# Kernel optimization log

Hardware: AMD Instinct MI355X
Metric: run time of the kernel (lower is better)

## Reference

```python
import jax, jax.numpy as jnp
import numpy as np

TEMPERATURE = 0.07
EPS = 1e-8          # torch cosine_similarity norm clamp
DIAG_FILL = 9e-15   # value masked_fill'ed onto the diagonal BEFORE temperature scaling


def setup_inputs() -> dict:
    key = jax.random.key(0)
    N, D = 16384, 128
    feats = jax.random.normal(key, (N, D), dtype=jnp.float32)
    # unique labels: required for the original torch code's broadcast
    # (-cos_sim[pos_mask] must have exactly N elements)
    labels = jnp.arange(N, dtype=jnp.int32).reshape(N, 1)
    return {"feats": feats, "labels": labels}


def reference(feats, labels):
    # cosine similarity matrix: normalize rows once, then a single GEMM
    norm = jnp.maximum(jnp.linalg.norm(feats, axis=-1, keepdims=True), EPS)
    f = feats / norm
    cos_sim = f @ f.T                                   # [N, N]

    N = cos_sim.shape[0]
    eye = jnp.eye(N, dtype=bool)
    cos_sim = jnp.where(eye, DIAG_FILL, cos_sim)        # masked_fill_(self_mask, 9e-15)
    cos_sim = cos_sim / TEMPERATURE

    pos_mask = labels == labels.T                       # [N, N] bool, one True per row
    # cos_sim[pos_mask] with exactly one positive per row == masked row-sum
    pos = jnp.sum(jnp.where(pos_mask, cos_sim, 0.0), axis=-1)  # [N]

    nll = -pos + jax.nn.logsumexp(cos_sim, axis=-1)     # [N]
    return jnp.mean(nll)
```

## Files before the change

kernel.cpp:

```cpp
#include <hip/hip_runtime.h>
#include <hip/hip_bf16.h>
#include <stdint.h>

typedef __attribute__((ext_vector_type(8))) short short8;
typedef __attribute__((ext_vector_type(4))) float f32x4;

#define N_ROWS 16384
#define DIM 128

constexpr float ALPHA = 4.5398160f;
constexpr float POSC = 1.2857143e-13f;

__device__ __forceinline__ void gload_lds16(const void* g, void* lds) {
  __builtin_amdgcn_global_load_lds(
      (const __attribute__((address_space(1))) void*)(uintptr_t)g,
      (__attribute__((address_space(3))) void*)(uintptr_t)lds,
      16, 0, 0);
}

__global__ void normalize_kernel(const float* __restrict__ feats,
                                 unsigned short* __restrict__ G,
                                 float* __restrict__ rowsum) {
  const int tid  = threadIdx.x;
  const int lane = tid & 63;
  const int row  = blockIdx.x * 4 + (tid >> 6);

  const float2 v = *(const float2*)(feats + (size_t)row * DIM + lane * 2);
  float ss = v.x * v.x + v.y * v.y;
#pragma unroll
  for (int m = 1; m < 64; m <<= 1) ss += __shfl_xor(ss, m);
  const float sc = ALPHA / fmaxf(sqrtf(ss), 1e-8f);

  __hip_bfloat16 h0 = __float2bfloat16(v.x * sc);
  __hip_bfloat16 h1 = __float2bfloat16(v.y * sc);
  unsigned int packed = (unsigned int)(*(unsigned short*)&h0) |
                        ((unsigned int)(*(unsigned short*)&h1) << 16);
  *(unsigned int*)(G + (size_t)row * DIM + lane * 2) = packed;

  if (blockIdx.x < 64) rowsum[blockIdx.x * 256 + tid] = 0.f;
}

__global__ __launch_bounds__(256, 2) void simclr_lse_kernel(
    const unsigned short* __restrict__ G, float* __restrict__ rowsum) {
  const int tid  = threadIdx.x;
  const int lane = tid & 63;
  const int w    = tid >> 6;
  const int wr   = w >> 1;
  const int wc   = w & 1;
  const int c    = lane & 15;
  const int q    = lane >> 4;

  const int rt      = blockIdx.x & 127;
  const int seg     = blockIdx.x >> 7;
  const int rowBase = rt * 128;

  __shared__ __align__(16) unsigned short Bbuf[128 * 128];
  __shared__ float ldsRow[128];

  if (tid < 128) ldsRow[tid] = 0.f;

  short8 afrag[4][4];
  {
    const short* Gs = (const short*)G;
    const int rbw = rowBase + wr * 64;
#pragma unroll
    for (int tr = 0; tr < 4; ++tr)
#pragma unroll
      for (int ks = 0; ks < 4; ++ks) {
        const int row = rbw + tr * 16 + c;
        afrag[tr][ks] = *(const short8*)(Gs + (size_t)row * DIM + ks * 32 + q * 8);
      }
  }

  unsigned boff[4][4];
#pragma unroll
  for (int tc = 0; tc < 4; ++tc)
#pragma unroll
    for (int ks = 0; ks < 4; ++ks) {
      const int col = wc * 64 + tc * 16 + c;
      const int kc  = ks * 4 + q;
      boff[tc][ks] = (unsigned)((col * 16 + (kc ^ c)) * 16);
    }

  unsigned goff[8];
#pragma unroll
  for (int t = 0; t < 8; ++t) {
    const int cidx = t * 256 + tid;
    const int col  = cidx >> 4;
    const int kc   = (cidx & 15) ^ (col & 15);
    goff[t] = (unsigned)(col * DIM + kc * 8);
  }

  float rs[4][4];
#pragma unroll
  for (int tr = 0; tr < 4; ++tr)
#pragma unroll
    for (int r = 0; r < 4; ++r) rs[tr][r] = 0.f;

  const f32x4 zero4 = {0.f, 0.f, 0.f, 0.f};
  const char* bbase = (const char*)Bbuf;

  for (int ch = 0; ch < 32; ++ch) {
    const int cb = seg * 4096 + ch * 128;
    __syncthreads();
    {
      const unsigned short* gsrc = G + (size_t)cb * DIM;
#pragma unroll
      for (int t = 0; t < 8; ++t)
        gload_lds16(gsrc + goff[t], (void*)(Bbuf + (size_t)(t * 256 + w * 64) * 8));
    }
    __syncthreads();

    f32x4 acc[4][4];
#pragma unroll
    for (int ks = 0; ks < 4; ++ks) {
      short8 bfr[4];
#pragma unroll
      for (int tc = 0; tc < 4; ++tc)
        bfr[tc] = *(const short8*)(bbase + boff[tc][ks]);
#pragma unroll
      for (int tr = 0; tr < 4; ++tr)
#pragma unroll
        for (int tc = 0; tc < 4; ++tc) {
          if (ks == 0)
            acc[tr][tc] = __builtin_amdgcn_mfma_f32_16x16x32_bf16(
                afrag[tr][0], bfr[tc], zero4, 0, 0, 0);
          else
            acc[tr][tc] = __builtin_amdgcn_mfma_f32_16x16x32_bf16(
                afrag[tr][ks], bfr[tc], acc[tr][tc], 0, 0, 0);
        }
    }

    if (cb == rowBase && wr == wc) {
#pragma unroll
      for (int tr = 0; tr < 4; ++tr)
#pragma unroll
        for (int r = 0; r < 4; ++r)
          if (c == q * 4 + r) acc[tr][tr][r] = 0.f;
    }

#pragma unroll
    for (int tr = 0; tr < 4; ++tr)
#pragma unroll
      for (int r = 0; r < 4; ++r) {
        float s = rs[tr][r];
#pragma unroll
        for (int tc = 0; tc < 4; ++tc)
          s += __builtin_amdgcn_exp2f(acc[tr][tc][r]);
        rs[tr][r] = s;
      }
  }

#pragma unroll
  for (int tr = 0; tr < 4; ++tr)
#pragma unroll
    for (int r = 0; r < 4; ++r) {
      float v = rs[tr][r];
      v += __shfl_xor(v, 1);
      v += __shfl_xor(v, 2);
      v += __shfl_xor(v, 4);
      v += __shfl_xor(v, 8);
      rs[tr][r] = v;
    }
  if (c == 0) {
#pragma unroll
    for (int tr = 0; tr < 4; ++tr)
#pragma unroll
      for (int r = 0; r < 4; ++r)
        atomicAdd(&ldsRow[wr * 64 + tr * 16 + q * 4 + r], rs[tr][r]);
  }
  __syncthreads();
  if (tid < 128) atomicAdd(&rowsum[rowBase + tid], ldsRow[tid]);
}

__global__ void finalize_kernel(const float* __restrict__ rowsum,
                                float* __restrict__ out) {
  const int tid = threadIdx.x;
  float local = 0.f;
  for (int i = tid; i < N_ROWS; i += 1024) local += logf(rowsum[i]);
#pragma unroll
  for (int m = 1; m < 64; m <<= 1) local += __shfl_xor(local, m);
  __shared__ float part[16];
  if ((tid & 63) == 0) part[tid >> 6] = local;
  __syncthreads();
  if (tid == 0) {
    float s = 0.f;
#pragma unroll
    for (int i = 0; i < 16; ++i) s += part[i];
    out[0] = s / (float)N_ROWS - POSC;
  }
}

extern "C" void kernel_launch(void* const* d_in, const int* in_sizes, int n_in,
                              void* d_out, int out_size, void* d_ws, size_t ws_size,
                              hipStream_t stream) {
  (void)in_sizes; (void)n_in; (void)out_size; (void)ws_size;
  const float* feats = (const float*)d_in[0];
  unsigned short* G = (unsigned short*)d_ws;
  float* rowsum = (float*)((char*)d_ws + (size_t)N_ROWS * DIM * 2);

  normalize_kernel<<<dim3(N_ROWS / 4), dim3(256), 0, stream>>>(feats, G, rowsum);
  simclr_lse_kernel<<<dim3(512), dim3(256), 0, stream>>>(G, rowsum);
  finalize_kernel<<<dim3(1), dim3(1024), 0, stream>>>(rowsum, d_out ? (float*)d_out : nullptr);
}
```

Before: 131.2 us.

## Exploit Gram symmetry with triangular tile scheduling and fuse finalize via last-block

Because the similarity matrix is symmetric, only upper-triangular 128x128 tiles are computed. Each off-diagonal tile's exponentials feed both row sums and column sums, which roughly halves the MFMA and exp work. Tiles are taken from a persistent grid through an atomic work counter in groups of four, and the A fragment is reused while the row tile stays the same. The separate finalize kernel is folded into the last finishing block using a completion counter, which removes a launch. This adds more atomics, extra column reductions through LDS, and a serial log-sum tail in a single block.

Result: slower. 362.2 us (+176.2%).

```diff
diff --git a/kernel.cpp b/kernel.cpp
--- a/kernel.cpp
+++ b/kernel.cpp
@@ -7,9 +7,13 @@
 
 #define N_ROWS 16384
 #define DIM 128
+#define NT 128
+#define TOTAL_CHUNKS 8256
+#define TRI_BLOCKS 1024
 
 constexpr float ALPHA = 4.5398160f;
-constexpr float POSC = 1.2857143e-13f;
+constexpr float POSC  = 1.2857143e-13f;
+constexpr float LN2   = 0.69314718056f;
 
 __device__ __forceinline__ void gload_lds16(const void* g, void* lds) {
   __builtin_amdgcn_global_load_lds(
@@ -20,7 +24,8 @@
 
 __global__ void normalize_kernel(const float* __restrict__ feats,
                                  unsigned short* __restrict__ G,
-                                 float* __restrict__ rowsum) {
+                                 float* __restrict__ rowsum,
+                                 unsigned int* __restrict__ cnts) {
   const int tid  = threadIdx.x;
   const int lane = tid & 63;
   const int row  = blockIdx.x * 4 + (tid >> 6);
@@ -38,49 +43,26 @@
   *(unsigned int*)(G + (size_t)row * DIM + lane * 2) = packed;
 
   if (blockIdx.x < 64) rowsum[blockIdx.x * 256 + tid] = 0.f;
-}
-
-__global__ __launch_bounds__(256, 2) void simclr_lse_kernel(
-    const unsigned short* __restrict__ G, float* __restrict__ rowsum) {
+  if (blockIdx.x == 0 && tid < 2) cnts[tid] = 0u;
+}
+
+__global__ __launch_bounds__(256, 3) void simclr_tri_kernel(
+    const unsigned short* __restrict__ G, float* __restrict__ rowsum,
+    unsigned int* __restrict__ cnts, float* __restrict__ out) {
   const int tid  = threadIdx.x;
   const int lane = tid & 63;
   const int w    = tid >> 6;
-  const int wr   = w >> 1;
-  const int wc   = w & 1;
   const int c    = lane & 15;
   const int q    = lane >> 4;
 
-  const int rt      = blockIdx.x & 127;
-  const int seg     = blockIdx.x >> 7;
-  const int rowBase = rt * 128;
-
   __shared__ __align__(16) unsigned short Bbuf[128 * 128];
-  __shared__ float ldsRow[128];
-
-  if (tid < 128) ldsRow[tid] = 0.f;
-
-  short8 afrag[4][4];
-  {
-    const short* Gs = (const short*)G;
-    const int rbw = rowBase + wr * 64;
-#pragma unroll
-    for (int tr = 0; tr < 4; ++tr)
-#pragma unroll
-      for (int ks = 0; ks < 4; ++ks) {
-        const int row = rbw + tr * 16 + c;
-        afrag[tr][ks] = *(const short8*)(Gs + (size_t)row * DIM + ks * 32 + q * 8);
-      }
-  }
-
-  unsigned boff[4][4];
-#pragma unroll
-  for (int tc = 0; tc < 4; ++tc)
-#pragma unroll
-    for (int ks = 0; ks < 4; ++ks) {
-      const int col = wc * 64 + tc * 16 + c;
-      const int kc  = ks * 4 + q;
-      boff[tc][ks] = (unsigned)((col * 16 + (kc ^ c)) * 16);
-    }
+  __shared__ float ldsCol[2][128];
+  __shared__ int gS[2];
+  __shared__ int finFlag;
+
+  ((float*)ldsCol)[tid] = 0.f;
+  if (tid == 0) gS[0] = (int)atomicAdd(&cnts[0], 1u) * 4;
+  __syncthreads();
 
   unsigned goff[8];
 #pragma unroll
@@ -90,104 +72,172 @@
     const int kc   = (cidx & 15) ^ (col & 15);
     goff[t] = (unsigned)(col * DIM + kc * 8);
   }
-
-  float rs[4][4];
-#pragma unroll
-  for (int tr = 0; tr < 4; ++tr)
-#pragma unroll
-    for (int r = 0; r < 4; ++r) rs[tr][r] = 0.f;
-
+  unsigned colb[8];
+#pragma unroll
+  for (int tc = 0; tc < 8; ++tc) colb[tc] = (unsigned)((tc * 16 + c) * 256);
+
+  const short* Gs = (const short*)G;
+  const char*  bb = (const char*)Bbuf;
   const f32x4 zero4 = {0.f, 0.f, 0.f, 0.f};
-  const char* bbase = (const char*)Bbuf;
-
-  for (int ch = 0; ch < 32; ++ch) {
-    const int cb = seg * 4096 + ch * 128;
+
+  short8 afrag[2][4];
+  float rs[2][4];
+  int cur_rt = -1, prev_ct = -1;
+  int it = 0, grp = 0;
+
+  while (true) {
+    const int gbase = gS[grp & 1];
+    if (gbase >= TOTAL_CHUNKS) break;
+
+#pragma unroll 1
+    for (int j = 0; j < 4; ++j) {
+      const int g = gbase + j;
+      const int p  = (int)((unsigned)g / 129u);
+      const int qq = g - p * 129;
+      const int rt = (qq < 128 - p) ? p : 127 - p;
+      const int ct = (qq < 128 - p) ? p + qq : qq - 1;
+      const bool offd = (rt != ct);
+
+      __syncthreads();
+      if (j == 0 && tid == 0) gS[(grp + 1) & 1] = (int)atomicAdd(&cnts[0], 1u) * 4;
+
+      if (prev_ct >= 0 && tid < 128) {
+        const int pf = (it + 1) & 1;
+        atomicAdd(&rowsum[prev_ct * 128 + tid], ldsCol[pf][tid]);
+        ldsCol[pf][tid] = 0.f;
+      }
+
+      const bool newA = (rt != cur_rt);
+      if (newA && cur_rt >= 0) {
+#pragma unroll
+        for (int tr = 0; tr < 2; ++tr)
+#pragma unroll
+          for (int r = 0; r < 4; ++r) {
+            float v = rs[tr][r];
+            v += __shfl_xor(v, 1); v += __shfl_xor(v, 2);
+            v += __shfl_xor(v, 4); v += __shfl_xor(v, 8);
+            if (c == 0)
+              atomicAdd(&rowsum[cur_rt * 128 + w * 32 + tr * 16 + q * 4 + r], v);
+          }
+      }
+
+      {
+        const unsigned short* gsrc = G + ((size_t)ct << 14);
+#pragma unroll
+        for (int t = 0; t < 8; ++t)
+          gload_lds16(gsrc + goff[t], (void*)(Bbuf + (size_t)(t * 256 + w * 64) * 8));
+      }
+      if (newA) {
+        const short* ap = Gs + ((size_t)(rt * 128 + w * 32 + c) << 7) + q * 8;
+#pragma unroll
+        for (int tr = 0; tr < 2; ++tr)
+#pragma unroll
+          for (int ks = 0; ks < 4; ++ks)
+            afrag[tr][ks] = *(const short8*)(ap + tr * 16 * 128 + ks * 32);
+#pragma unroll
+        for (int tr = 0; tr < 2; ++tr)
+#pragma unroll
+          for (int r = 0; r < 4; ++r) rs[tr][r] = 0.f;
+        cur_rt = rt;
+      }
+      __syncthreads();
+
+      f32x4 acc[2][8];
+#pragma unroll
+      for (int ks = 0; ks < 4; ++ks) {
+        const unsigned kx = (unsigned)(((ks * 4 + q) ^ c) * 16);
+#pragma unroll
+        for (int half = 0; half < 2; ++half) {
+          short8 bfr[4];
+#pragma unroll
+          for (int jj = 0; jj < 4; ++jj)
+            bfr[jj] = *(const short8*)(bb + colb[half * 4 + jj] + kx);
+#pragma unroll
+          for (int tr = 0; tr < 2; ++tr)
+#pragma unroll
+            for (int jj = 0; jj < 4; ++jj) {
+              const int tc = half * 4 + jj;
+              acc[tr][tc] = __builtin_amdgcn_mfma_f32_16x16x32_bf16(
+                  afrag[tr][ks], bfr[jj],
+                  (ks == 0) ? zero4 : acc[tr][tc], 0, 0, 0);
+            }
+        }
+      }
+
+      if (!offd) {
+#pragma unroll
+        for (int tr = 0; tr < 2; ++tr)
+#pragma unroll
+          for (int r = 0; r < 4; ++r)
+            if (c == q * 4 + r) acc[tr][w * 2 + tr][r] = 0.f;
+      }
+
+      float cs[8];
+#pragma unroll
+      for (int tc = 0; tc < 8; ++tc) cs[tc] = 0.f;
+#pragma unroll
+      for (int tr = 0; tr < 2; ++tr)
+#pragma unroll
+        for (int tc = 0; tc < 8; ++tc) {
+          const float e0 = __builtin_amdgcn_exp2f(acc[tr][tc][0]);
+          const float e1 = __builtin_amdgcn_exp2f(acc[tr][tc][1]);
+          const float e2 = __builtin_amdgcn_exp2f(acc[tr][tc][2]);
+          const float e3 = __builtin_amdgcn_exp2f(acc[tr][tc][3]);
+          rs[tr][0] += e0; rs[tr][1] += e1; rs[tr][2] += e2; rs[tr][3] += e3;
+          cs[tc] += (e0 + e1) + (e2 + e3);
+        }
+      if (offd) {
+#pragma unroll
+        for (int tc = 0; tc < 8; ++tc) {
+          float v = cs[tc];
+          v += __shfl_xor(v, 16); v += __shfl_xor(v, 32);
+          if (q == 0) atomicAdd(&ldsCol[it & 1][tc * 16 + c], v);
+        }
+      }
+      prev_ct = offd ? ct : -1;
+      ++it;
+    }
+    ++grp;
+  }
+
+  __syncthreads();
+  if (prev_ct >= 0 && tid < 128)
+    atomicAdd(&rowsum[prev_ct * 128 + tid], ldsCol[(it + 1) & 1][tid]);
+  if (cur_rt >= 0) {
+#pragma unroll
+    for (int tr = 0; tr < 2; ++tr)
+#pragma unroll
+      for (int r = 0; r < 4; ++r) {
+        float v = rs[tr][r];
+        v += __shfl_xor(v, 1); v += __shfl_xor(v, 2);
+        v += __shfl_xor(v, 4); v += __shfl_xor(v, 8);
+        if (c == 0)
+          atomicAdd(&rowsum[cur_rt * 128 + w * 32 + tr * 16 + q * 4 + r], v);
+      }
+  }
+
+  __syncthreads();
+  if (tid == 0) {
+    __threadfence();
+    const unsigned old = atomicAdd(&cnts[1], 1u);
+    finFlag = (old == (unsigned)gridDim.x - 1u) ? 1 : 0;
+  }
+  __syncthreads();
+  if (finFlag) {
+    float lsum = 0.f;
+    for (int i = tid; i < N_ROWS; i += 256) {
+      const float v = __hip_atomic_load(&rowsum[i], __ATOMIC_RELAXED,
+                                        __HIP_MEMORY_SCOPE_AGENT);
+      lsum += __builtin_amdgcn_logf(v);
+    }
+#pragma unroll
+    for (int m = 1; m < 64; m <<= 1) lsum += __shfl_xor(lsum, m);
+    if (lane == 0) ldsCol[0][w] = lsum;
     __syncthreads();
-    {
-      const unsigned short* gsrc = G + (size_t)cb * DIM;
-#pragma unroll
-      for (int t = 0; t < 8; ++t)
-        gload_lds16(gsrc + goff[t], (void*)(Bbuf + (size_t)(t * 256 + w * 64) * 8));
+    if (tid == 0) {
+      const float s = ldsCol[0][0] + ldsCol[0][1] + ldsCol[0][2] + ldsCol[0][3];
+      out[0] = s * LN2 / (float)N_ROWS - POSC;
     }
-    __syncthreads();
-
-    f32x4 acc[4][4];
-#pragma unroll
-    for (int ks = 0; ks < 4; ++ks) {
-      short8 bfr[4];
-#pragma unroll
-      for (int tc = 0; tc < 4; ++tc)
-        bfr[tc] = *(const short8*)(bbase + boff[tc][ks]);
-#pragma unroll
-      for (int tr = 0; tr < 4; ++tr)
-#pragma unroll
-        for (int tc = 0; tc < 4; ++tc) {
-          if (ks == 0)
-            acc[tr][tc] = __builtin_amdgcn_mfma_f32_16x16x32_bf16(
-                afrag[tr][0], bfr[tc], zero4, 0, 0, 0);
-          else
-            acc[tr][tc] = __builtin_amdgcn_mfma_f32_16x16x32_bf16(
-                afrag[tr][ks], bfr[tc], acc[tr][tc], 0, 0, 0);
-        }
-    }
-
-    if (cb == rowBase && wr == wc) {
-#pragma unroll
-      for (int tr = 0; tr < 4; ++tr)
-#pragma unroll
-        for (int r = 0; r < 4; ++r)
-          if (c == q * 4 + r) acc[tr][tr][r] = 0.f;
-    }
-
-#pragma unroll
-    for (int tr = 0; tr < 4; ++tr)
-#pragma unroll
-      for (int r = 0; r < 4; ++r) {
-        float s = rs[tr][r];
-#pragma unroll
-        for (int tc = 0; tc < 4; ++tc)
-          s += __builtin_amdgcn_exp2f(acc[tr][tc][r]);
-        rs[tr][r] = s;
-      }
-  }
-
-#pragma unroll
-  for (int tr = 0; tr < 4; ++tr)
-#pragma unroll
-    for (int r = 0; r < 4; ++r) {
-      float v = rs[tr][r];
-      v += __shfl_xor(v, 1);
-      v += __shfl_xor(v, 2);
-      v += __shfl_xor(v, 4);
-      v += __shfl_xor(v, 8);
-      rs[tr][r] = v;
-    }
-  if (c == 0) {
-#pragma unroll
-    for (int tr = 0; tr < 4; ++tr)
-#pragma unroll
-      for (int r = 0; r < 4; ++r)
-        atomicAdd(&ldsRow[wr * 64 + tr * 16 + q * 4 + r], rs[tr][r]);
-  }
-  __syncthreads();
-  if (tid < 128) atomicAdd(&rowsum[rowBase + tid], ldsRow[tid]);
-}
-
-__global__ void finalize_kernel(const float* __restrict__ rowsum,
-                                float* __restrict__ out) {
-  const int tid = threadIdx.x;
-  float local = 0.f;
-  for (int i = tid; i < N_ROWS; i += 1024) local += logf(rowsum[i]);
-#pragma unroll
-  for (int m = 1; m < 64; m <<= 1) local += __shfl_xor(local, m);
-  __shared__ float part[16];
-  if ((tid & 63) == 0) part[tid >> 6] = local;
-  __syncthreads();
-  if (tid == 0) {
-    float s = 0.f;
-#pragma unroll
-    for (int i = 0; i < 16; ++i) s += part[i];
-    out[0] = s / (float)N_ROWS - POSC;
   }
 }
 
@@ -198,8 +248,10 @@
   const float* feats = (const float*)d_in[0];
   unsigned short* G = (unsigned short*)d_ws;
   float* rowsum = (float*)((char*)d_ws + (size_t)N_ROWS * DIM * 2);
-
-  normalize_kernel<<<dim3(N_ROWS / 4), dim3(256), 0, stream>>>(feats, G, rowsum);
-  simclr_lse_kernel<<<dim3(512), dim3(256), 0, stream>>>(G, rowsum);
-  finalize_kernel<<<dim3(1), dim3(1024), 0, stream>>>(rowsum, d_out ? (float*)d_out : nullptr);
-}
+  unsigned int* cnts =
+      (unsigned int*)((char*)d_ws + (size_t)N_ROWS * DIM * 2 + N_ROWS * 4);
+
+  normalize_kernel<<<dim3(N_ROWS / 4), dim3(256), 0, stream>>>(feats, G, rowsum, cnts);
+  simclr_tri_kernel<<<dim3(TRI_BLOCKS), dim3(256), 0, stream>>>(
+      G, rowsum, cnts, (float*)d_out);
+}
```
